# Optimization experiments

Hardware: AMD Instinct MI355X
Metric: run time of the kernel (lower is better)

The kernel has to match this reference:

```python
import jax, jax.numpy as jnp
import numpy as np

N_NODES = 100000
N_EDGES = 1600000
F_IN_N = 64
F_IN_E = 64
F_OUT_N = 64
F_OUT_E = 64


def setup_inputs() -> dict:
    key = jax.random.key(0)
    ks = jax.random.split(key, 10)
    nfeats = jax.random.normal(ks[0], (N_NODES, F_IN_N), dtype=jnp.float32)
    efeats = jax.random.normal(ks[1], (N_EDGES, F_IN_E), dtype=jnp.float32)
    src = jax.random.randint(ks[2], (N_EDGES,), 0, N_NODES, dtype=jnp.int32)
    dst = jax.random.randint(ks[3], (N_EDGES,), 0, N_NODES, dtype=jnp.int32)
    s = 0.05
    W_node = jax.random.normal(ks[4], (F_OUT_N, F_IN_N), dtype=jnp.float32) * s
    b_node = jnp.zeros((F_OUT_N,), dtype=jnp.float32)
    W_ni = jax.random.normal(ks[5], (F_OUT_E, F_IN_N), dtype=jnp.float32) * s
    W_nj = jax.random.normal(ks[6], (F_OUT_E, F_IN_N), dtype=jnp.float32) * s
    W_fij = jax.random.normal(ks[7], (F_OUT_E, F_IN_E), dtype=jnp.float32) * s
    bias = jnp.zeros((F_OUT_E,), dtype=jnp.float32)
    return {"nfeats": nfeats, "efeats": efeats, "src": src, "dst": dst,
            "W_node": W_node, "b_node": b_node, "W_ni": W_ni, "W_nj": W_nj,
            "W_fij": W_fij, "bias": bias}


def reference(nfeats, efeats, src, dst, W_node, b_node, W_ni, W_nj, W_fij, bias):
    # edge update: leaky_relu(f_ni[src] + f_nj[dst] + f_fij + bias)
    f_ni = nfeats @ W_ni.T        # [N, Fe]
    f_nj = nfeats @ W_nj.T        # [N, Fe]
    f_fij = efeats @ W_fij.T      # [E, Fe]
    f_out = jax.nn.leaky_relu(f_ni[src] + f_nj[dst] + f_fij + bias, negative_slope=0.01)
    # node update: mean over in-edges of transformed source features
    h = nfeats @ W_node.T + b_node                      # [N, Fn]
    msg_sum = jax.ops.segment_sum(h[src], dst, num_segments=N_NODES)   # [N, Fn]
    deg = jax.ops.segment_sum(jnp.ones((src.shape[0],), dtype=h.dtype), dst,
                              num_segments=N_NODES)
    h_out = msg_sum / jnp.maximum(deg, 1.0)[:, None]    # 0 for isolated nodes
    return (h_out, f_out)
```

## Files before the change

### kernel.cpp

```cpp
#include <hip/hip_runtime.h>

#define NN 100000
#define NE 1600000
#define F 64
#define NSB ((NN + 255) / 256)
#define NTB ((NN + 127) / 128)

typedef float f32x4 __attribute__((ext_vector_type(4)));
typedef float f32x2 __attribute__((ext_vector_type(2)));
typedef short bf16x8 __attribute__((ext_vector_type(8)));

__device__ inline unsigned short f2bf(float f) {
    unsigned u = __builtin_bit_cast(unsigned, f);
    u = (u + 0x7fffu + ((u >> 16) & 1u)) >> 16;
    return (unsigned short)u;
}
__device__ inline float bf2f(unsigned short b) { return __builtin_bit_cast(float, (unsigned)b << 16); }
__device__ inline float bflo(unsigned u) { return __builtin_bit_cast(float, u << 16); }
__device__ inline float bfhi(unsigned u) { return __builtin_bit_cast(float, u & 0xffff0000u); }

__device__ inline bf16x8 pack8(const f32x4 v0, const f32x4 v1) {
    bf16x8 pk;
    pk[0] = (short)f2bf(v0[0]); pk[1] = (short)f2bf(v0[1]);
    pk[2] = (short)f2bf(v0[2]); pk[3] = (short)f2bf(v0[3]);
    pk[4] = (short)f2bf(v1[0]); pk[5] = (short)f2bf(v1[1]);
    pk[6] = (short)f2bf(v1[2]); pk[7] = (short)f2bf(v1[3]);
    return pk;
}

__device__ inline bf16x8 wfrag(const float* __restrict__ Wp, int c, int kslot) {
    const f32x4* g = reinterpret_cast<const f32x4*>(Wp + c * F + kslot * 8);
    return pack8(g[0], g[1]);
}

__global__ __launch_bounds__(256, 2) void node_kernel(
    const float* __restrict__ nfeats,
    const float* __restrict__ W_node, const float* __restrict__ b_node,
    const float* __restrict__ W_ni,   const float* __restrict__ W_nj,
    unsigned short* __restrict__ f_ni16, unsigned short* __restrict__ f_nj16,
    unsigned short* __restrict__ h16, int* __restrict__ counts)
{
    __shared__ bf16x8 As8[128 * 8];
    float* Df = reinterpret_cast<float*>(As8);

    const int t = threadIdx.x;
    const int w = t >> 6, lane = t & 63;
    const int tile0 = blockIdx.x * 128;
    const int m = blockIdx.y;

    if (m == 0 && t < 128 && tile0 + t < NN) counts[tile0 + t] = 0;

    const float* Wp = (m == 0) ? W_ni : (m == 1) ? W_nj : W_node;
    unsigned short* outp = (m == 0) ? f_ni16 : (m == 1) ? f_nj16 : h16;

    {
        const f32x4* gsrc = reinterpret_cast<const f32x4*>(nfeats + (size_t)tile0 * F);
#pragma unroll
        for (int i = 0; i < 4; ++i) {
            const int c = w * 256 + i * 64 + lane;
            const int row = c >> 3, slot = c & 7;
            f32x4 v0 = f32x4{0.f, 0.f, 0.f, 0.f}, v1 = f32x4{0.f, 0.f, 0.f, 0.f};
            if (tile0 + row < NN) { v0 = gsrc[2 * c]; v1 = gsrc[2 * c + 1]; }
            As8[row * 8 + (slot ^ (row & 7))] = pack8(v0, v1);
        }
    }
    __builtin_amdgcn_wave_barrier();

    bf16x8 af[2][2];
#pragma unroll
    for (int mt = 0; mt < 2; ++mt)
#pragma unroll
        for (int ks = 0; ks < 2; ++ks) {
            const int row = w * 32 + mt * 16 + (lane & 15);
            const int kslot = ks * 4 + (lane >> 4);
            af[mt][ks] = As8[row * 8 + (kslot ^ (row & 7))];
        }
    __builtin_amdgcn_wave_barrier();

#pragma unroll
    for (int half = 0; half < 2; ++half) {
        bf16x8 bfr[2][2];
#pragma unroll
        for (int ntl = 0; ntl < 2; ++ntl)
#pragma unroll
            for (int ks = 0; ks < 2; ++ks)
                bfr[ntl][ks] = wfrag(Wp, (half * 2 + ntl) * 16 + (lane & 15), ks * 4 + (lane >> 4));

        f32x4 acc[2][2];
#pragma unroll
        for (int mt = 0; mt < 2; ++mt)
#pragma unroll
            for (int ntl = 0; ntl < 2; ++ntl) acc[mt][ntl] = f32x4{0.f, 0.f, 0.f, 0.f};
#pragma unroll
        for (int ks = 0; ks < 2; ++ks)
#pragma unroll
            for (int mt = 0; mt < 2; ++mt)
#pragma unroll
                for (int ntl = 0; ntl < 2; ++ntl)
                    acc[mt][ntl] = __builtin_amdgcn_mfma_f32_16x16x32_bf16(
                        af[mt][ks], bfr[ntl][ks], acc[mt][ntl], 0, 0, 0);

#pragma unroll
        for (int mt = 0; mt < 2; ++mt)
#pragma unroll
            for (int ntl = 0; ntl < 2; ++ntl)
#pragma unroll
                for (int r = 0; r < 4; ++r) {
                    const int row = w * 32 + mt * 16 + (lane >> 4) * 4 + r;
                    const int col = ntl * 16 + (lane & 15);
                    float v = acc[mt][ntl][r];
                    if (m == 2) v += b_node[half * 32 + col];
                    Df[row * 32 + ((col + row) & 31)] = v;
                }
        __builtin_amdgcn_wave_barrier();

#pragma unroll
        for (int i = 0; i < 2; ++i) {
            const int idx = i * 64 + lane;
            const int row = w * 32 + (idx >> 2);
            const int c8 = (idx & 3) << 3;
            if (tile0 + row < NN) {
                const float* b = Df + row * 32;
                uint4 pk;
                unsigned u[4];
#pragma unroll
                for (int p = 0; p < 4; ++p) {
                    const unsigned lo = f2bf(b[(c8 + 2 * p + 0 + row) & 31]);
                    const unsigned hi = f2bf(b[(c8 + 2 * p + 1 + row) & 31]);
                    u[p] = lo | (hi << 16);
                }
                pk.x = u[0]; pk.y = u[1]; pk.z = u[2]; pk.w = u[3];
                *reinterpret_cast<uint4*>(outp + (size_t)(tile0 + row) * F + half * 32 + c8) = pk;
            }
        }
        __builtin_amdgcn_wave_barrier();
    }
}

__global__ __launch_bounds__(256, 2) void edge_kernel(
    const float* __restrict__ efeats,
    const int* __restrict__ src, const int* __restrict__ dst,
    const unsigned short* __restrict__ f_ni16, const unsigned short* __restrict__ f_nj16,
    const float* __restrict__ W_fij, const float* __restrict__ bias,
    float* __restrict__ f_out, int* __restrict__ counts)
{
    __shared__ bf16x8 As8[256 * 8];
    float* Df = reinterpret_cast<float*>(As8);

    const int t = threadIdx.x;
    const int w = t >> 6, lane = t & 63;
    const int tile0 = blockIdx.x * 256;
    const int e = tile0 + t;
    const int s = src[e], d = dst[e];

    const uint4* gi = reinterpret_cast<const uint4*>(f_ni16 + (size_t)s * F);
    const uint4* gj = reinterpret_cast<const uint4*>(f_nj16 + (size_t)d * F);

    uint4 vni[4], vnj[4];
#pragma unroll
    for (int i = 0; i < 4; ++i) { vni[i] = gi[i]; vnj[i] = gj[i]; }

    {
        const f32x4* gsrc = reinterpret_cast<const f32x4*>(efeats + (size_t)tile0 * F);
#pragma unroll
        for (int i = 0; i < 8; ++i) {
            const int c = w * 512 + i * 64 + lane;
            const int row = c >> 3, slot = c & 7;
            const f32x4 v0 = __builtin_nontemporal_load(gsrc + 2 * c);
            const f32x4 v1 = __builtin_nontemporal_load(gsrc + 2 * c + 1);
            As8[row * 8 + (slot ^ (row & 7))] = pack8(v0, v1);
        }
    }
    atomicAdd(&counts[d], 1);
    __builtin_amdgcn_wave_barrier();

    bf16x8 af[4][2];
#pragma unroll
    for (int mt = 0; mt < 4; ++mt)
#pragma unroll
        for (int ks = 0; ks < 2; ++ks) {
            const int row = w * 64 + mt * 16 + (lane & 15);
            const int kslot = ks * 4 + (lane >> 4);
            af[mt][ks] = As8[row * 8 + (kslot ^ (row & 7))];
        }
    bf16x8 bfr[2][2];
#pragma unroll
    for (int ntl = 0; ntl < 2; ++ntl)
#pragma unroll
        for (int ks = 0; ks < 2; ++ks)
            bfr[ntl][ks] = wfrag(W_fij, ntl * 16 + (lane & 15), ks * 4 + (lane >> 4));

    f32x4 acc[4][2];
#pragma unroll
    for (int mt = 0; mt < 4; ++mt)
#pragma unroll
        for (int ntl = 0; ntl < 2; ++ntl) acc[mt][ntl] = f32x4{0.f, 0.f, 0.f, 0.f};
#pragma unroll
    for (int ks = 0; ks < 2; ++ks)
#pragma unroll
        for (int mt = 0; mt < 4; ++mt)
#pragma unroll
            for (int ntl = 0; ntl < 2; ++ntl)
                acc[mt][ntl] = __builtin_amdgcn_mfma_f32_16x16x32_bf16(
                    af[mt][ks], bfr[ntl][ks], acc[mt][ntl], 0, 0, 0);

    __builtin_amdgcn_wave_barrier();

    f32x4* gout = reinterpret_cast<f32x4*>(f_out + (size_t)tile0 * F);

#pragma unroll
    for (int mt = 0; mt < 4; ++mt)
#pragma unroll
        for (int ntl = 0; ntl < 2; ++ntl)
#pragma unroll
            for (int r = 0; r < 4; ++r) {
                const int row = w * 64 + mt * 16 + (lane >> 4) * 4 + r;
                const int col = ntl * 16 + (lane & 15);
                Df[row * 32 + ((col + row) & 31)] = acc[mt][ntl][r];
            }
    __builtin_amdgcn_wave_barrier();

    {
        float* rb = Df + t * 32;
#pragma unroll
        for (int c = 0; c < 32; ++c) {
            float v = rb[(c + t) & 31];
            const unsigned wi = vni[c >> 3][(c >> 1) & 3];
            const unsigned wj = vnj[c >> 3][(c >> 1) & 3];
            v += (c & 1) ? bfhi(wi) : bflo(wi);
            v += (c & 1) ? bfhi(wj) : bflo(wj);
            v += bias[c];
            v = (v > 0.f) ? v : 0.01f * v;
            rb[(c + t) & 31] = v;
        }
    }
    uint4 nni[4], nnj[4];
#pragma unroll
    for (int i = 0; i < 4; ++i) { nni[i] = gi[4 + i]; nnj[i] = gj[4 + i]; }
    __builtin_amdgcn_wave_barrier();

#pragma unroll
    for (int i = 0; i < 8; ++i) {
        const int idx = i * 64 + lane;
        const int row = w * 64 + (idx >> 3);
        const int c4 = (idx & 7) << 2;
        const float* b = Df + row * 32;
        f32x4 v;
        v[0] = b[(c4 + 0 + row) & 31];
        v[1] = b[(c4 + 1 + row) & 31];
        v[2] = b[(c4 + 2 + row) & 31];
        v[3] = b[(c4 + 3 + row) & 31];
        __builtin_nontemporal_store(v, gout + row * 16 + (idx & 7));
    }
    __builtin_amdgcn_wave_barrier();

#pragma unroll
    for (int ntl = 0; ntl < 2; ++ntl)
#pragma unroll
        for (int ks = 0; ks < 2; ++ks)
            bfr[ntl][ks] = wfrag(W_fij, (2 + ntl) * 16 + (lane & 15), ks * 4 + (lane >> 4));
#pragma unroll
    for (int mt = 0; mt < 4; ++mt)
#pragma unroll
        for (int ntl = 0; ntl < 2; ++ntl) acc[mt][ntl] = f32x4{0.f, 0.f, 0.f, 0.f};
#pragma unroll
    for (int ks = 0; ks < 2; ++ks)
#pragma unroll
        for (int mt = 0; mt < 4; ++mt)
#pragma unroll
            for (int ntl = 0; ntl < 2; ++ntl)
                acc[mt][ntl] = __builtin_amdgcn_mfma_f32_16x16x32_bf16(
                    af[mt][ks], bfr[ntl][ks], acc[mt][ntl], 0, 0, 0);

#pragma unroll
    for (int mt = 0; mt < 4; ++mt)
#pragma unroll
        for (int ntl = 0; ntl < 2; ++ntl)
#pragma unroll
            for (int r = 0; r < 4; ++r) {
                const int row = w * 64 + mt * 16 + (lane >> 4) * 4 + r;
                const int col = ntl * 16 + (lane & 15);
                Df[row * 32 + ((col + row) & 31)] = acc[mt][ntl][r];
            }
    __builtin_amdgcn_wave_barrier();
    {
        float* rb = Df + t * 32;
#pragma unroll
        for (int c = 0; c < 32; ++c) {
            float v = rb[(c + t) & 31];
            const unsigned wi = nni[c >> 3][(c >> 1) & 3];
            const unsigned wj = nnj[c >> 3][(c >> 1) & 3];
            v += (c & 1) ? bfhi(wi) : bflo(wi);
            v += (c & 1) ? bfhi(wj) : bflo(wj);
            v += bias[32 + c];
            v = (v > 0.f) ? v : 0.01f * v;
            rb[(c + t) & 31] = v;
        }
    }
    __builtin_amdgcn_wave_barrier();
#pragma unroll
    for (int i = 0; i < 8; ++i) {
        const int idx = i * 64 + lane;
        const int row = w * 64 + (idx >> 3);
        const int c4 = (idx & 7) << 2;
        const float* b = Df + row * 32;
        f32x4 v;
        v[0] = b[(c4 + 0 + row) & 31];
        v[1] = b[(c4 + 1 + row) & 31];
        v[2] = b[(c4 + 2 + row) & 31];
        v[3] = b[(c4 + 3 + row) & 31];
        __builtin_nontemporal_store(v, gout + row * 16 + 8 + (idx & 7));
    }
}

__global__ __launch_bounds__(256) void scan1_kernel(
    const int* __restrict__ counts, int* __restrict__ offsets, int* __restrict__ blocksums)
{
    __shared__ int sd[256];
    const int t = threadIdx.x;
    const int i = blockIdx.x * 256 + t;
    const int v = (i < NN) ? counts[i] : 0;
    sd[t] = v;
    __syncthreads();
#pragma unroll
    for (int off = 1; off < 256; off <<= 1) {
        const int x = (t >= off) ? sd[t - off] : 0;
        __syncthreads();
        sd[t] += x;
        __syncthreads();
    }
    if (i < NN) offsets[i] = sd[t] - v;
    if (t == 255) blocksums[blockIdx.x] = sd[255];
}

__global__ __launch_bounds__(512) void scan2_kernel(
    const int* __restrict__ blocksums, int* __restrict__ blockpref)
{
    __shared__ int sd[512];
    const int t = threadIdx.x;
    const int v = (t < NSB) ? blocksums[t] : 0;
    sd[t] = v;
    __syncthreads();
#pragma unroll
    for (int off = 1; off < 512; off <<= 1) {
        const int x = (t >= off) ? sd[t - off] : 0;
        __syncthreads();
        sd[t] += x;
        __syncthreads();
    }
    if (t < NSB) blockpref[t] = sd[t] - v;
}

__global__ __launch_bounds__(256) void scan3_kernel(
    int* __restrict__ offsets, const int* __restrict__ blockpref, int* __restrict__ cursor)
{
    const int i = blockIdx.x * 256 + threadIdx.x;
    if (i < NN) {
        const int o = offsets[i] + blockpref[blockIdx.x];
        offsets[i] = o;
        cursor[i] = o;
    }
    if (i == 0) offsets[NN] = NE;
}

__global__ __launch_bounds__(256) void place_kernel(
    const int* __restrict__ src, const int* __restrict__ dst,
    int* __restrict__ cursor, int* __restrict__ eidx)
{
    const int e = blockIdx.x * 256 + threadIdx.x;
    if (e >= NE) return;
    const int pos = atomicAdd(&cursor[dst[e]], 1);
    eidx[pos] = src[e];
}

__global__ __launch_bounds__(256) void gather_kernel(
    const unsigned short* __restrict__ h16, const int* __restrict__ offsets,
    const int* __restrict__ eidx, float* __restrict__ h_out)
{
    const int n = blockIdx.x * 4 + (threadIdx.x >> 6);
    const int lane = threadIdx.x & 63;
    if (n >= NN) return;
    const int beg = offsets[n], end = offsets[n + 1];
    const int colp = (lane & 31) * 2;
    const int sel = lane >> 5;
    float a0 = 0.f, a1 = 0.f;
    int k = beg;
    for (; k + 4 <= end; k += 4) {
        const int e0 = eidx[k + sel];
        const int e1 = eidx[k + 2 + sel];
        const unsigned u0 = *reinterpret_cast<const unsigned*>(h16 + (size_t)e0 * F + colp);
        const unsigned u1 = *reinterpret_cast<const unsigned*>(h16 + (size_t)e1 * F + colp);
        a0 += bflo(u0) + bflo(u1);
        a1 += bfhi(u0) + bfhi(u1);
    }
    for (; k + 2 <= end; k += 2) {
        const int e0 = eidx[k + sel];
        const unsigned u0 = *reinterpret_cast<const unsigned*>(h16 + (size_t)e0 * F + colp);
        a0 += bflo(u0);
        a1 += bfhi(u0);
    }
    if (k < end && sel == 0) {
        const int e0 = eidx[k];
        const unsigned u0 = *reinterpret_cast<const unsigned*>(h16 + (size_t)e0 * F + colp);
        a0 += bflo(u0);
        a1 += bfhi(u0);
    }
    a0 += __shfl_xor(a0, 32, 64);
    a1 += __shfl_xor(a1, 32, 64);
    if (sel == 0) {
        const float dg = fmaxf((float)(end - beg), 1.0f);
        f32x2 o;
        o[0] = a0 / dg;
        o[1] = a1 / dg;
        __builtin_nontemporal_store(o, reinterpret_cast<f32x2*>(h_out + (size_t)n * F + colp));
    }
}

extern "C" void kernel_launch(void* const* d_in, const int* in_sizes, int n_in,
                              void* d_out, int out_size, void* d_ws, size_t ws_size,
                              hipStream_t stream)
{
    const float* nfeats = (const float*)d_in[0];
    const float* efeats = (const float*)d_in[1];
    const int*   src    = (const int*)  d_in[2];
    const int*   dst    = (const int*)  d_in[3];
    const float* W_node = (const float*)d_in[4];
    const float* b_node = (const float*)d_in[5];
    const float* W_ni   = (const float*)d_in[6];
    const float* W_nj   = (const float*)d_in[7];
    const float* W_fij  = (const float*)d_in[8];
    const float* bias   = (const float*)d_in[9];

    float* h_out = (float*)d_out;
    float* f_out = (float*)d_out + (size_t)NN * F;

    unsigned short* f_ni16 = (unsigned short*)d_ws;
    unsigned short* f_nj16 = f_ni16 + (size_t)NN * F;
    unsigned short* h16    = f_nj16 + (size_t)NN * F;
    int*   offsets = (int*)(h16 + (size_t)NN * F);
    int*   cursor  = offsets + (NN + 1);
    int*   counts  = cursor + NN;
    int*   eidx    = counts + NN;
    int*   blocksums = eidx + NE;
    int*   blockpref = blocksums + NSB;
    const size_t need = ((size_t)3 * NN * F) * sizeof(unsigned short)
                      + ((size_t)(3 * NN + 1) + NE + 2 * NSB) * sizeof(int);
    if (ws_size < need) return;

    node_kernel<<<dim3(NTB, 3), 256, 0, stream>>>(nfeats, W_node, b_node, W_ni, W_nj,
                                                  f_ni16, f_nj16, h16, counts);
    edge_kernel<<<NE / 256, 256, 0, stream>>>(efeats, src, dst, f_ni16, f_nj16, W_fij, bias,
                                              f_out, counts);
    scan1_kernel<<<NSB, 256, 0, stream>>>(counts, offsets, blocksums);
    scan2_kernel<<<1, 512, 0, stream>>>(blocksums, blockpref);
    scan3_kernel<<<NSB, 256, 0, stream>>>(offsets, blockpref, cursor);
    place_kernel<<<(NE + 255) / 256, 256, 0, stream>>>(src, dst, cursor, eidx);
    gather_kernel<<<(NN + 3) / 4, 256, 0, stream>>>(h16, offsets, eidx, h_out);
}
```

Before: 461.6 us.

## Load A fragments directly from global and stage W_fij in shared memory

Both kernels now read the activation fragments for the MFMA straight from global memory into registers in MFMA layout, rather than staging them through a swizzled LDS tile first. The edge kernel also converts W_fij to bf16 once per block into a swizzled LDS buffer, so each wave no longer re-reads and re-converts the weights from global memory for both column halves. This removes an LDS round-trip and the per-wave weight conversion, but it adds a block-wide barrier and makes the global loads less coalesced (each lane reads 32 bytes from a different row). The separate Df buffer also increases LDS usage per block.

```diff
diff --git a/kernel.cpp b/kernel.cpp
--- a/kernel.cpp
+++ b/kernel.cpp
@@ -40,9 +40,7 @@
     unsigned short* __restrict__ f_ni16, unsigned short* __restrict__ f_nj16,
     unsigned short* __restrict__ h16, int* __restrict__ counts)
 {
-    __shared__ bf16x8 As8[128 * 8];
-    float* Df = reinterpret_cast<float*>(As8);
-
+    __shared__ float Df[128 * 32];
     const int t = threadIdx.x;
     const int w = t >> 6, lane = t & 63;
     const int tile0 = blockIdx.x * 128;
@@ -53,29 +51,20 @@
     const float* Wp = (m == 0) ? W_ni : (m == 1) ? W_nj : W_node;
     unsigned short* outp = (m == 0) ? f_ni16 : (m == 1) ? f_nj16 : h16;
 
-    {
-        const f32x4* gsrc = reinterpret_cast<const f32x4*>(nfeats + (size_t)tile0 * F);
-#pragma unroll
-        for (int i = 0; i < 4; ++i) {
-            const int c = w * 256 + i * 64 + lane;
-            const int row = c >> 3, slot = c & 7;
+    bf16x8 af[2][2];
+#pragma unroll
+    for (int mt = 0; mt < 2; ++mt)
+#pragma unroll
+        for (int ks = 0; ks < 2; ++ks) {
+            const int rg = tile0 + w * 32 + mt * 16 + (lane & 15);
+            const int koff = (ks * 4 + (lane >> 4)) * 8;
             f32x4 v0 = f32x4{0.f, 0.f, 0.f, 0.f}, v1 = f32x4{0.f, 0.f, 0.f, 0.f};
-            if (tile0 + row < NN) { v0 = gsrc[2 * c]; v1 = gsrc[2 * c + 1]; }
-            As8[row * 8 + (slot ^ (row & 7))] = pack8(v0, v1);
-        }
-    }
-    __builtin_amdgcn_wave_barrier();
-
-    bf16x8 af[2][2];
-#pragma unroll
-    for (int mt = 0; mt < 2; ++mt)
-#pragma unroll
-        for (int ks = 0; ks < 2; ++ks) {
-            const int row = w * 32 + mt * 16 + (lane & 15);
-            const int kslot = ks * 4 + (lane >> 4);
-            af[mt][ks] = As8[row * 8 + (kslot ^ (row & 7))];
-        }
-    __builtin_amdgcn_wave_barrier();
+            if (rg < NN) {
+                const f32x4* g = reinterpret_cast<const f32x4*>(nfeats + (size_t)rg * F + koff);
+                v0 = g[0]; v1 = g[1];
+            }
+            af[mt][ks] = pack8(v0, v1);
+        }
 
 #pragma unroll
     for (int half = 0; half < 2; ++half) {
@@ -144,9 +133,8 @@
     const float* __restrict__ W_fij, const float* __restrict__ bias,
     float* __restrict__ f_out, int* __restrict__ counts)
 {
-    __shared__ bf16x8 As8[256 * 8];
-    float* Df = reinterpret_cast<float*>(As8);
-
+    __shared__ bf16x8 Ws8[64 * 8];
+    __shared__ float Df[256 * 32];
     const int t = threadIdx.x;
     const int w = t >> 6, lane = t & 63;
     const int tile0 = blockIdx.x * 256;
@@ -161,35 +149,41 @@
     for (int i = 0; i < 4; ++i) { vni[i] = gi[i]; vnj[i] = gj[i]; }
 
     {
-        const f32x4* gsrc = reinterpret_cast<const f32x4*>(efeats + (size_t)tile0 * F);
-#pragma unroll
-        for (int i = 0; i < 8; ++i) {
-            const int c = w * 512 + i * 64 + lane;
+        const f32x4* gw = reinterpret_cast<const f32x4*>(W_fij);
+#pragma unroll
+        for (int i = 0; i < 2; ++i) {
+            const int c = i * 256 + t;
             const int row = c >> 3, slot = c & 7;
-            const f32x4 v0 = __builtin_nontemporal_load(gsrc + 2 * c);
-            const f32x4 v1 = __builtin_nontemporal_load(gsrc + 2 * c + 1);
-            As8[row * 8 + (slot ^ (row & 7))] = pack8(v0, v1);
-        }
+            Ws8[row * 8 + (slot ^ (row & 7))] = pack8(gw[2 * c], gw[2 * c + 1]);
+        }
+    }
+    bf16x8 af[4][2];
+    {
+        const float* ab = efeats + (size_t)(tile0 + w * 64) * F;
+#pragma unroll
+        for (int mt = 0; mt < 4; ++mt)
+#pragma unroll
+            for (int ks = 0; ks < 2; ++ks) {
+                const int rl = mt * 16 + (lane & 15);
+                const int koff = (ks * 4 + (lane >> 4)) * 8;
+                const f32x4* g = reinterpret_cast<const f32x4*>(ab + rl * F + koff);
+                const f32x4 v0 = __builtin_nontemporal_load(g);
+                const f32x4 v1 = __builtin_nontemporal_load(g + 1);
+                af[mt][ks] = pack8(v0, v1);
+            }
     }
     atomicAdd(&counts[d], 1);
-    __builtin_amdgcn_wave_barrier();
-
-    bf16x8 af[4][2];
-#pragma unroll
-    for (int mt = 0; mt < 4; ++mt)
+    __syncthreads();
+
+    bf16x8 bfr[2][2];
+#pragma unroll
+    for (int ntl = 0; ntl < 2; ++ntl)
 #pragma unroll
         for (int ks = 0; ks < 2; ++ks) {
-            const int row = w * 64 + mt * 16 + (lane & 15);
+            const int c = ntl * 16 + (lane & 15);
             const int kslot = ks * 4 + (lane >> 4);
-            af[mt][ks] = As8[row * 8 + (kslot ^ (row & 7))];
-        }
-    bf16x8 bfr[2][2];
-#pragma unroll
-    for (int ntl = 0; ntl < 2; ++ntl)
-#pragma unroll
-        for (int ks = 0; ks < 2; ++ks)
-            bfr[ntl][ks] = wfrag(W_fij, ntl * 16 + (lane & 15), ks * 4 + (lane >> 4));
-
+            bfr[ntl][ks] = Ws8[c * 8 + (kslot ^ (c & 7))];
+        }
     f32x4 acc[4][2];
 #pragma unroll
     for (int mt = 0; mt < 4; ++mt)
@@ -203,8 +197,6 @@
             for (int ntl = 0; ntl < 2; ++ntl)
                 acc[mt][ntl] = __builtin_amdgcn_mfma_f32_16x16x32_bf16(
                     af[mt][ks], bfr[ntl][ks], acc[mt][ntl], 0, 0, 0);
-
-    __builtin_amdgcn_wave_barrier();
 
     f32x4* gout = reinterpret_cast<f32x4*>(f_out + (size_t)tile0 * F);
 
@@ -257,8 +249,11 @@
 #pragma unroll
     for (int ntl = 0; ntl < 2; ++ntl)
 #pragma unroll
-        for (int ks = 0; ks < 2; ++ks)
-            bfr[ntl][ks] = wfrag(W_fij, (2 + ntl) * 16 + (lane & 15), ks * 4 + (lane >> 4));
+        for (int ks = 0; ks < 2; ++ks) {
+            const int c = (2 + ntl) * 16 + (lane & 15);
+            const int kslot = ks * 4 + (lane >> 4);
+            bfr[ntl][ks] = Ws8[c * 8 + (kslot ^ (c & 7))];
+        }
 #pragma unroll
     for (int mt = 0; mt < 4; ++mt)
 #pragma unroll
```

Measured after the change: 455.2 us. Within noise of the previous version (-1.4%).
